# Performance work log

Hardware: AMD Instinct MI355X
Metric: run time of the kernel (lower is better)

Reference implementation:

```python
import jax, jax.numpy as jnp
import numpy as np

NEG_SLOPE = 0.2


def gat_conv(x, src, dst, W, asrc, adst, b):
    """Single-head PyG-style GATConv with self-loops.
    x: [N, din], src/dst: [E] int, W: [din, d], asrc/adst: [d], b: [d]."""
    N = x.shape[0]
    h = x @ W  # [N, d]
    alpha_s = h @ asrc  # [N]
    alpha_d = h @ adst  # [N]
    # add self loops so every node has at least one incoming edge
    loop = jnp.arange(N, dtype=src.dtype)
    srcf = jnp.concatenate([src, loop])
    dstf = jnp.concatenate([dst, loop])
    e = jax.nn.leaky_relu(alpha_s[srcf] + alpha_d[dstf], NEG_SLOPE)  # [E+N]
    m = jax.ops.segment_max(e, dstf, num_segments=N)
    ex = jnp.exp(e - m[dstf])
    denom = jax.ops.segment_sum(ex, dstf, num_segments=N)
    alpha = ex / denom[dstf]
    out = jax.ops.segment_sum(h[srcf] * alpha[:, None], dstf, num_segments=N)
    return out + b


def sdgnn_forward(x, edges, Wg, a_src, a_dst, bg, W1, b1, W2, b2):
    L = Wg.shape[0]
    R = Wg.shape[1]
    for l in range(L):
        feats = [x]
        for r in range(R):
            feats.append(gat_conv(x, edges[r, 0], edges[r, 1],
                                  Wg[l, r], a_src[l, r], a_dst[l, r], bg[l, r]))
        combined = jnp.concatenate(feats, axis=1)  # [N, 5*d]
        x = jnp.tanh(combined @ W1[l] + b1[l]) @ W2[l] + b2[l]
    return x


def setup_inputs() -> dict:
    key = jax.random.key(0)
    ks = jax.random.split(key, 8)
    N, D, E, L, R = 100000, 64, 1000000, 2, 4
    scale = 0.15  # ~kaiming for d=64
    x = jax.random.normal(ks[0], (N, D), dtype=jnp.float32)
    edges = jax.random.randint(ks[1], (R, 2, E), 0, N, dtype=jnp.int64)
    Wg = jax.random.normal(ks[2], (L, R, D, D), dtype=jnp.float32) * scale
    a_src = jax.random.normal(ks[3], (L, R, D), dtype=jnp.float32) * scale
    a_dst = jax.random.normal(ks[4], (L, R, D), dtype=jnp.float32) * scale
    bg = jnp.zeros((L, R, D), dtype=jnp.float32)
    W1 = jax.random.normal(ks[5], (L, 5 * D, D), dtype=jnp.float32) * 0.08
    b1 = jnp.zeros((L, D), dtype=jnp.float32)
    W2 = jax.random.normal(ks[6], (L, D, D), dtype=jnp.float32) * scale
    b2 = jnp.zeros((L, D), dtype=jnp.float32)
    return {"x": x, "edges": edges, "Wg": Wg, "a_src": a_src, "a_dst": a_dst,
            "bg": bg, "W1": W1, "b1": b1, "W2": W2, "b2": b2}


def reference(x, edges, Wg, a_src, a_dst, bg, W1, b1, W2, b2):
    return sdgnn_forward(x, edges, Wg, a_src, a_dst, bg, W1, b1, W2, b2)
```

## Files before the change

kernel.cpp:

```cpp
#include <hip/hip_runtime.h>
#include <hip/hip_bf16.h>
#include <math.h>

#define DD 64
#define RREL 4
#define LLAY 2
#define NEG_SLOPE 0.2f
#define EPB 4096
#define BSH 10
#define BSZ 1024

typedef __attribute__((ext_vector_type(8))) short short8;
typedef __attribute__((ext_vector_type(4))) short short4v;
typedef __attribute__((ext_vector_type(4))) float float4v;

__device__ __forceinline__ float lrelu(float x) { return x > 0.f ? x : NEG_SLOPE * x; }

__device__ __forceinline__ unsigned short f2bf(float f) {
    unsigned int u = __float_as_uint(f);
    return (unsigned short)((u + 0x7FFFu + ((u >> 16) & 1u)) >> 16);
}
__device__ __forceinline__ float bf2f(unsigned short u) {
    return __uint_as_float((unsigned int)u << 16);
}

__global__ void k_wvec(const float* __restrict__ Wg, const float* __restrict__ asrc,
                       const float* __restrict__ adst, float* __restrict__ wsrc,
                       float* __restrict__ wdst) {
    int idx = blockIdx.x * blockDim.x + threadIdx.x;
    if (idx >= LLAY * RREL * DD) return;
    int k = idx & 63;
    int lr = idx >> 6;
    const float* W = Wg + (size_t)lr * DD * DD;
    const float* as = asrc + lr * DD;
    const float* ad = adst + lr * DD;
    float s1 = 0.f, s2 = 0.f;
#pragma unroll
    for (int j = 0; j < DD; j++) {
        float w = W[k * DD + j];
        s1 += w * as[j];
        s2 += w * ad[j];
    }
    wsrc[idx] = s1;
    wdst[idx] = s2;
}

__global__ void k_prep(const float* __restrict__ Wg, const float* __restrict__ W1,
                       const float* __restrict__ W2, unsigned short* __restrict__ WgT,
                       unsigned short* __restrict__ W1T, unsigned short* __restrict__ W2T) {
    int idx = blockIdx.x * blockDim.x + threadIdx.x;
    if (idx < 8 * 4096) {
        int lr = idx >> 12, rem = idx & 4095, n = rem >> 6, k = rem & 63;
        WgT[idx] = f2bf(Wg[(size_t)lr * 4096 + k * 64 + n]);
    } else if (idx < 32768 + 2 * 64 * 320) {
        int i = idx - 32768;
        int l = i / 20480, rem = i % 20480, n = rem / 320, kk = rem % 320;
        int src;
        if (kk < 64) src = kk;
        else {
            int r = (kk - 64) >> 6, f = (kk - 64) & 63;
            src = 64 + r * 64 + ((f & 3) * 16) + (f >> 2);
        }
        W1T[i] = f2bf(W1[(size_t)l * 20480 + src * 64 + n]);
    } else if (idx < 32768 + 40960 + 2 * 4096) {
        int i = idx - 73728;
        int l = i >> 12, rem = i & 4095, n = rem >> 6, k = rem & 63;
        W2T[i] = f2bf(W2[(size_t)l * 4096 + k * 64 + n]);
    }
}

__global__ void k_copy_x(const float* __restrict__ x, unsigned short* __restrict__ combined,
                         int N) {
    int i = blockIdx.x * blockDim.x + threadIdx.x;
    if (i >= N * 32) return;
    int row = i >> 5, c2 = i & 31;
    float2 v = *(const float2*)(x + (size_t)row * DD + c2 * 2);
    unsigned int p = (unsigned int)f2bf(v.x) | ((unsigned int)f2bf(v.y) << 16);
    *(unsigned int*)(combined + (size_t)row * 320 + c2 * 2) = p;
}

__global__ void k_zero(int* __restrict__ p, int n) {
    int i = blockIdx.x * blockDim.x + threadIdx.x;
    if (i < n) p[i] = 0;
}

__global__ __launch_bounds__(256) void k_bhist(const int* __restrict__ edges,
                                               int* __restrict__ btot, int E, int NB) {
    int r = blockIdx.y;
    int e0 = blockIdx.x * EPB;
    int t = threadIdx.x;
    __shared__ int lh[128];
    for (int i = t; i < 128; i += 256) lh[i] = 0;
    __syncthreads();
    const int* dstp = edges + (size_t)r * 2 * E + E;
#pragma unroll
    for (int i = 0; i < EPB / 256; i++) {
        int e = e0 + t + 256 * i;
        if (e < E) atomicAdd(&lh[dstp[e] >> BSH], 1);
    }
    __syncthreads();
    for (int i = t; i < NB; i += 256) {
        int c = lh[i];
        if (c) atomicAdd(&btot[r * NB + i], c);
    }
}

__global__ void k_bscan(const int* __restrict__ btot, int* __restrict__ bucketoff,
                        int* __restrict__ bpos, int* __restrict__ csr_ptr, int N, int E, int NB) {
    int r = threadIdx.x;
    if (r >= RREL) return;
    int run = 0;
    for (int b = 0; b < NB; b++) {
        bucketoff[r * (NB + 1) + b] = run;
        bpos[r * NB + b] = run;
        run += btot[r * NB + b];
    }
    bucketoff[r * (NB + 1) + NB] = run;
    csr_ptr[(size_t)r * (N + 1) + N] = E;
}

__global__ __launch_bounds__(256) void k_binscatter(const int* __restrict__ edges,
                                                    int* __restrict__ bpos,
                                                    unsigned int* __restrict__ packed, int E,
                                                    int NB) {
    int r = blockIdx.y;
    int e0 = blockIdx.x * EPB;
    int t = threadIdx.x;
    __shared__ int lh[128], lbase[128];
    for (int i = t; i < 128; i += 256) lh[i] = 0;
    __syncthreads();
    const int* srcp = edges + (size_t)r * 2 * E;
    const int* dstp = srcp + E;
    int md[EPB / 256], ms[EPB / 256];
#pragma unroll
    for (int i = 0; i < EPB / 256; i++) {
        int e = e0 + t + 256 * i;
        int d = -1, s = 0;
        if (e < E) {
            d = dstp[e];
            s = srcp[e];
            atomicAdd(&lh[d >> BSH], 1);
        }
        md[i] = d;
        ms[i] = s;
    }
    __syncthreads();
    for (int i = t; i < NB; i += 256) {
        int c = lh[i];
        lbase[i] = c ? atomicAdd(&bpos[r * NB + i], c) : 0;
        lh[i] = 0;
    }
    __syncthreads();
#pragma unroll
    for (int i = 0; i < EPB / 256; i++) {
        if (md[i] >= 0) {
            int b = md[i] >> BSH;
            int p = lbase[b] + atomicAdd(&lh[b], 1);
            packed[(size_t)r * E + p] =
                ((unsigned int)(md[i] & (BSZ - 1)) << 17) | (unsigned int)ms[i];
        }
    }
}

__global__ __launch_bounds__(256) void k_bucket_sort(const unsigned int* __restrict__ packed,
                                                     const int* __restrict__ bucketoff,
                                                     int* __restrict__ csr_ptr,
                                                     int* __restrict__ csr_src, int N, int E,
                                                     int NB) {
    int r = blockIdx.y, b = blockIdx.x;
    int t = threadIdx.x;
    __shared__ int pos[BSZ];
    __shared__ int tsum[256];
    int base = bucketoff[r * (NB + 1) + b];
    int cnt = bucketoff[r * (NB + 1) + b + 1] - base;
    const unsigned int* pk = packed + (size_t)r * E + base;
    for (int i = t; i < BSZ; i += 256) pos[i] = 0;
    __syncthreads();
    for (int i = t; i < cnt; i += 256) atomicAdd(&pos[pk[i] >> 17], 1);
    __syncthreads();
    int v[4];
    int s = 0;
#pragma unroll
    for (int i = 0; i < 4; i++) {
        v[i] = pos[t * 4 + i];
        s += v[i];
    }
    tsum[t] = s;
    __syncthreads();
    for (int off = 1; off < 256; off <<= 1) {
        int add = (t >= off) ? tsum[t - off] : 0;
        __syncthreads();
        tsum[t] += add;
        __syncthreads();
    }
    int run = tsum[t] - s;
    __syncthreads();
#pragma unroll
    for (int i = 0; i < 4; i++) {
        int node_l = t * 4 + i;
        pos[node_l] = run;
        int node = b * BSZ + node_l;
        if (node < N) csr_ptr[(size_t)r * (N + 1) + node] = base + run;
        run += v[i];
    }
    __syncthreads();
    for (int i = t; i < cnt; i += 256) {
        unsigned int p = pk[i];
        int d = p >> 17;
        int sidx = p & 0x1FFFF;
        int loc = atomicAdd(&pos[d], 1);
        csr_src[(size_t)r * E + base + loc] = sidx;
    }
}

__global__ __launch_bounds__(256) void k_elog(const int* __restrict__ csr_src,
                                              const float* __restrict__ as4,
                                              float* __restrict__ e_edge, int E, int N) {
    int r = blockIdx.y;
    const int* cs = csr_src + (size_t)r * E;
    const float* as_ = as4 + (size_t)r * N;
    float* ee = e_edge + (size_t)r * E;
    int base = blockIdx.x * 1024 + threadIdx.x;
    int s[4];
#pragma unroll
    for (int u = 0; u < 4; u++) {
        int e = base + u * 256;
        s[u] = (e < E) ? cs[e] : 0;
    }
#pragma unroll
    for (int u = 0; u < 4; u++) {
        int e = base + u * 256;
        if (e < E) ee[e] = as_[s[u]];
    }
}


__global__ __launch_bounds__(256, 3) void k_hgemm(const unsigned short* __restrict__ X,
                                                  const unsigned short* __restrict__ WgTl,
                                                  const float* __restrict__ wsrcl,
                                                  const float* __restrict__ wdstl,
                                                  unsigned short* __restrict__ h4,
                                                  float* __restrict__ as4,
                                                  float* __restrict__ ad4, int N) {
    __shared__ __align__(16) unsigned short Xb[256][72];
    __shared__ __align__(16) unsigned short Wb[64][72];
    __shared__ float wsS[4][64], wdS[4][64];
    int tid = threadIdx.x, wave = tid >> 6, lane = tid & 63;
    int l15 = lane & 15, q = lane >> 4;
    int row0 = blockIdx.x * 256;
#pragma unroll
    for (int i = 0; i < 8; i++) {
        int f = tid + 256 * i;
        int rr = f >> 3, seg = f & 7;
        int grow = row0 + rr;
        short8 v = (short8){0, 0, 0, 0, 0, 0, 0, 0};
        if (grow < N) v = *(const short8*)(X + (size_t)grow * 320 + seg * 8);
        *(short8*)&Xb[rr][seg * 8] = v;
    }
    wsS[tid >> 6][tid & 63] = wsrcl[tid];
    wdS[tid >> 6][tid & 63] = wdstl[tid];
    __syncthreads();
    short8 afr[4][2];
#pragma unroll
    for (int mt = 0; mt < 4; mt++)
#pragma unroll
        for (int ks = 0; ks < 2; ks++)
            afr[mt][ks] = *(const short8*)&Xb[wave * 64 + mt * 16 + l15][ks * 32 + q * 8];
    {
        int grow = row0 + tid;
        float s[4] = {0.f, 0.f, 0.f, 0.f}, d[4] = {0.f, 0.f, 0.f, 0.f};
#pragma unroll
        for (int seg = 0; seg < 8; seg++) {
            short8 v = *(const short8*)&Xb[tid][seg * 8];
#pragma unroll
            for (int j = 0; j < 8; j++) {
                float xv = bf2f((unsigned short)v[j]);
                int k = seg * 8 + j;
#pragma unroll
                for (int r = 0; r < 4; r++) {
                    s[r] += xv * wsS[r][k];
                    d[r] += xv * wdS[r][k];
                }
            }
        }
        if (grow < N) {
#pragma unroll
            for (int r = 0; r < 4; r++) {
                as4[(size_t)r * N + grow] = s[r];
                ad4[(size_t)r * N + grow] = d[r];
            }
        }
    }
    for (int r = 0; r < 4; r++) {
        __syncthreads();
#pragma unroll
        for (int i = 0; i < 2; i++) {
            int f = tid + 256 * i;
            int n = f >> 3, seg = f & 7;
            *(short8*)&Wb[n][seg * 8] = *(const short8*)(WgTl + r * 4096 + n * 64 + seg * 8);
        }
        __syncthreads();
        short8 bfr[4][2];
#pragma unroll
        for (int nt = 0; nt < 4; nt++)
#pragma unroll
            for (int ks = 0; ks < 2; ks++)
                bfr[nt][ks] = *(const short8*)&Wb[nt * 16 + l15][ks * 32 + q * 8];
        float4v acc[4][4];
#pragma unroll
        for (int mt = 0; mt < 4; mt++)
#pragma unroll
            for (int nt = 0; nt < 4; nt++) acc[mt][nt] = (float4v){0.f, 0.f, 0.f, 0.f};
#pragma unroll
        for (int mt = 0; mt < 4; mt++)
#pragma unroll
            for (int nt = 0; nt < 4; nt++) {
                acc[mt][nt] = __builtin_amdgcn_mfma_f32_16x16x32_bf16(afr[mt][0], bfr[nt][0],
                                                                     acc[mt][nt], 0, 0, 0);
                acc[mt][nt] = __builtin_amdgcn_mfma_f32_16x16x32_bf16(afr[mt][1], bfr[nt][1],
                                                                     acc[mt][nt], 0, 0, 0);
            }
        unsigned short* hr = h4 + (size_t)r * N * 64;
#pragma unroll
        for (int mt = 0; mt < 4; mt++) {
            int rowb = row0 + wave * 64 + mt * 16 + q * 4;
#pragma unroll
            for (int reg = 0; reg < 4; reg++) {
                int row = rowb + reg;
                if (row < N) {
                    short4v sv;
                    sv[0] = (short)f2bf(acc[mt][0][reg]);
                    sv[1] = (short)f2bf(acc[mt][1][reg]);
                    sv[2] = (short)f2bf(acc[mt][2][reg]);
                    sv[3] = (short)f2bf(acc[mt][3][reg]);
                    *(short4v*)&hr[(size_t)row * 64 + l15 * 4] = sv;
                }
            }
        }
    }
}

__global__ __launch_bounds__(256, 3) void k_w1gemm(const unsigned short* __restrict__ X,
                                                   const unsigned short* __restrict__ WT,
                                                   const float* __restrict__ bias,
                                                   unsigned short* __restrict__ Y, int N) {
    __shared__ __align__(16) unsigned short Xb[256][72];
    __shared__ __align__(16) unsigned short Wb[64][72];
    int tid = threadIdx.x, wave = tid >> 6, lane = tid & 63;
    int l15 = lane & 15, q = lane >> 4;
    int row0 = blockIdx.x * 256;
    float4v acc[4][4];
#pragma unroll
    for (int mt = 0; mt < 4; mt++)
#pragma unroll
        for (int nt = 0; nt < 4; nt++) acc[mt][nt] = (float4v){0.f, 0.f, 0.f, 0.f};
    for (int kc = 0; kc < 320; kc += 64) {
        __syncthreads();
#pragma unroll
        for (int i = 0; i < 8; i++) {
            int f = tid + 256 * i;
            int rr = f >> 3, seg = f & 7;
            int grow = row0 + rr;
            short8 v = (short8){0, 0, 0, 0, 0, 0, 0, 0};
            if (grow < N) v = *(const short8*)(X + (size_t)grow * 320 + kc + seg * 8);
            *(short8*)&Xb[rr][seg * 8] = v;
        }
#pragma unroll
        for (int i = 0; i < 2; i++) {
            int f = tid + 256 * i;
            int n = f >> 3, seg = f & 7;
            *(short8*)&Wb[n][seg * 8] = *(const short8*)(WT + n * 320 + kc + seg * 8);
        }
        __syncthreads();
        short8 bfr[4][2];
#pragma unroll
        for (int nt = 0; nt < 4; nt++)
#pragma unroll
            for (int ks = 0; ks < 2; ks++)
                bfr[nt][ks] = *(const short8*)&Wb[nt * 16 + l15][ks * 32 + q * 8];
#pragma unroll
        for (int mt = 0; mt < 4; mt++) {
            short8 a0 = *(const short8*)&Xb[wave * 64 + mt * 16 + l15][q * 8];
            short8 a1 = *(const short8*)&Xb[wave * 64 + mt * 16 + l15][32 + q * 8];
#pragma unroll
            for (int nt = 0; nt < 4; nt++) {
                acc[mt][nt] =
                    __builtin_amdgcn_mfma_f32_16x16x32_bf16(a0, bfr[nt][0], acc[mt][nt], 0, 0, 0);
                acc[mt][nt] =
                    __builtin_amdgcn_mfma_f32_16x16x32_bf16(a1, bfr[nt][1], acc[mt][nt], 0, 0, 0);
            }
        }
    }
#pragma unroll
    for (int mt = 0; mt < 4; mt++) {
        int rowb = row0 + wave * 64 + mt * 16 + q * 4;
#pragma unroll
        for (int reg = 0; reg < 4; reg++) {
            int row = rowb + reg;
            if (row < N) {
#pragma unroll
                for (int nt = 0; nt < 4; nt++) {
                    int n = nt * 16 + l15;
                    float v = tanhf(acc[mt][nt][reg] + bias[n]);
                    Y[(size_t)row * 64 + n] = f2bf(v);
                }
            }
        }
    }
}

template <bool BFOUT>
__global__ __launch_bounds__(256, 3) void k_w2gemm(const unsigned short* __restrict__ X,
                                                   const unsigned short* __restrict__ WT,
                                                   const float* __restrict__ bias,
                                                   unsigned short* __restrict__ Ybf,
                                                   float* __restrict__ Yf, int ldy, int N) {
    __shared__ __align__(16) unsigned short Xb[256][72];
    __shared__ __align__(16) unsigned short Wb[64][72];
    int tid = threadIdx.x, wave = tid >> 6, lane = tid & 63;
    int l15 = lane & 15, q = lane >> 4;
    int row0 = blockIdx.x * 256;
#pragma unroll
    for (int i = 0; i < 8; i++) {
        int f = tid + 256 * i;
        int rr = f >> 3, seg = f & 7;
        int grow = row0 + rr;
        short8 v = (short8){0, 0, 0, 0, 0, 0, 0, 0};
        if (grow < N) v = *(const short8*)(X + (size_t)grow * 64 + seg * 8);
        *(short8*)&Xb[rr][seg * 8] = v;
    }
#pragma unroll
    for (int i = 0; i < 2; i++) {
        int f = tid + 256 * i;
        int n = f >> 3, seg = f & 7;
        *(short8*)&Wb[n][seg * 8] = *(const short8*)(WT + n * 64 + seg * 8);
    }
    __syncthreads();
    short8 bfr[4][2];
#pragma unroll
    for (int nt = 0; nt < 4; nt++)
#pragma unroll
        for (int ks = 0; ks < 2; ks++)
            bfr[nt][ks] = *(const short8*)&Wb[nt * 16 + l15][ks * 32 + q * 8];
    float4v acc[4][4];
#pragma unroll
    for (int mt = 0; mt < 4; mt++)
#pragma unroll
        for (int nt = 0; nt < 4; nt++) acc[mt][nt] = (float4v){0.f, 0.f, 0.f, 0.f};
#pragma unroll
    for (int mt = 0; mt < 4; mt++) {
        short8 a0 = *(const short8*)&Xb[wave * 64 + mt * 16 + l15][q * 8];
        short8 a1 = *(const short8*)&Xb[wave * 64 + mt * 16 + l15][32 + q * 8];
#pragma unroll
        for (int nt = 0; nt < 4; nt++) {
            acc[mt][nt] =
                __builtin_amdgcn_mfma_f32_16x16x32_bf16(a0, bfr[nt][0], acc[mt][nt], 0, 0, 0);
            acc[mt][nt] =
                __builtin_amdgcn_mfma_f32_16x16x32_bf16(a1, bfr[nt][1], acc[mt][nt], 0, 0, 0);
        }
    }
#pragma unroll
    for (int mt = 0; mt < 4; mt++) {
        int rowb = row0 + wave * 64 + mt * 16 + q * 4;
#pragma unroll
        for (int reg = 0; reg < 4; reg++) {
            int row = rowb + reg;
            if (row < N) {
#pragma unroll
                for (int nt = 0; nt < 4; nt++) {
                    int n = nt * 16 + l15;
                    float v = acc[mt][nt][reg] + bias[n];
                    if (BFOUT)
                        Ybf[(size_t)row * ldy + n] = f2bf(v);
                    else
                        Yf[(size_t)row * ldy + n] = v;
                }
            }
        }
    }
}

__device__ void gat_node_fullwave(int node, const int* __restrict__ csr_ptr,
                                  const int* __restrict__ csr_src,
                                  const float* __restrict__ e_edge,
                                  const unsigned short* __restrict__ h,
                                  const float* __restrict__ as_,
                                  const float* __restrict__ ad_, float bgv,
                                  unsigned short* __restrict__ out, int ldo, int lane) {
    float adv = ad_[node];
    float e_self = lrelu(as_[node] + adv);
    int beg = csr_ptr[node], end = csr_ptr[node + 1];
    int cnt = end - beg;

    if (cnt <= 64) {
        int s = 0;
        float e_lane = -3.0e38f;
        if (lane < cnt) {
            s = csr_src[beg + lane];
            e_lane = lrelu(e_edge[beg + lane] + adv);
        }
        float m = fmaxf(e_lane, e_self);
#pragma unroll
        for (int off = 32; off; off >>= 1) m = fmaxf(m, __shfl_xor(m, off));
        float p = (lane < cnt) ? expf(e_lane - m) : 0.f;
        float ssum = p;
#pragma unroll
        for (int off = 32; off; off >>= 1) ssum += __shfl_xor(ssum, off);
        float p_self = expf(e_self - m);
        float inv = 1.f / (ssum + p_self);
        float alpha = p * inv;
        float acc = p_self * inv * bf2f(h[(size_t)node * DD + lane]);
        for (int j0 = 0; j0 < cnt; ++j0) {
            int ss = __shfl(s, j0);
            float aa = __shfl(alpha, j0);
            acc += aa * bf2f(h[(size_t)ss * DD + lane]);
        }
        out[(size_t)node * ldo + lane] = f2bf(acc + bgv);
        return;
    }

    float m = e_self;
    for (int j = beg + lane; j < end; j += 64) m = fmaxf(m, lrelu(e_edge[j] + adv));
#pragma unroll
    for (int off = 32; off; off >>= 1) m = fmaxf(m, __shfl_xor(m, off));
    float ssum = 0.f;
    for (int j = beg + lane; j < end; j += 64) ssum += expf(lrelu(e_edge[j] + adv) - m);
#pragma unroll
    for (int off = 32; off; off >>= 1) ssum += __shfl_xor(ssum, off);
    ssum += expf(e_self - m);
    float inv = 1.f / ssum;
    float acc = expf(e_self - m) * inv * bf2f(h[(size_t)node * DD + lane]);
    for (int j0 = beg; j0 < end; j0 += 64) {
        int j = j0 + lane;
        int s = 0;
        float alpha = 0.f;
        if (j < end) {
            s = csr_src[j];
            alpha = expf(lrelu(e_edge[j] + adv) - m) * inv;
        }
        int c = end - j0;
        if (c > 64) c = 64;
        for (int t = 0; t < c; ++t) {
            int ss = __shfl(s, t);
            float aa = __shfl(alpha, t);
            acc += aa * bf2f(h[(size_t)ss * DD + lane]);
        }
    }
    out[(size_t)node * ldo + lane] = f2bf(acc + bgv);
}

__global__ __launch_bounds__(256) void k_gat(const int* __restrict__ csr_ptr4,
                                             const int* __restrict__ csr_src4,
                                             const float* __restrict__ e_edge4,
                                             const unsigned short* __restrict__ h4,
                                             const float* __restrict__ as4,
                                             const float* __restrict__ ad4,
                                             const float* __restrict__ bg4,
                                             unsigned short* __restrict__ outbase, int ldo,
                                             int N, int E) {
    __shared__ int2 lsa[4][2][32];
    int lb = blockIdx.x;
    int r = (lb & 7) >> 1;
    int idx = ((lb >> 3) << 1) + (lb & 1);
    int wave = threadIdx.x >> 6, lane = threadIdx.x & 63;
    int half = lane >> 5, lh = lane & 31;
    int nodeA = idx * 8 + wave * 2;
    if (nodeA >= N) return;
    int node = nodeA + half;
    bool act = node < N;

    const int* csr_ptr = csr_ptr4 + (size_t)r * (N + 1);
    const int* csr_src = csr_src4 + (size_t)r * E;
    const float* e_edge = e_edge4 + (size_t)r * E;
    const unsigned short* h = h4 + (size_t)r * N * 64;
    const float* as_ = as4 + (size_t)r * N;
    const float* ad_ = ad4 + (size_t)r * N;
    const float* bg = bg4 + (size_t)r * DD;
    unsigned short* out = outbase + (size_t)64 * r;

    int beg = 0, cnt = 0;
    if (act) {
        beg = csr_ptr[node];
        cnt = csr_ptr[node + 1] - beg;
    }
    int vmax = __builtin_amdgcn_readfirstlane(max(cnt, __shfl_xor(cnt, 32)));

    if (vmax <= 32) {
        bool in = lh < cnt;
        int s = 0;
        float ev = 0.f;
        if (in) {
            s = csr_src[beg + lh];
            ev = e_edge[beg + lh];
        }
        float adv = act ? ad_[node] : 0.f;
        float e_self = act ? lrelu(as_[node] + adv) : 0.f;
        float p = in ? __expf(lrelu(ev + adv)) : 0.f;
        lsa[wave][half][lh] = make_int2(s, __float_as_int(p));
        float p_self = __expf(e_self);

        const char* hb = (const char*)h;
        unsigned lane4 = (unsigned)(lh << 2);
        unsigned int hvs = 0;
        if (act) hvs = *(const unsigned int*)(hb + (((unsigned)node) << 7) + lane4);

        float ax0 = 0.f, ay0 = 0.f, ax1 = 0.f, ay1 = 0.f;
        const int2* lp = &lsa[wave][half][0];
        for (int j0 = 0; j0 < vmax; j0 += 8) {
#pragma unroll
            for (int g = 0; g < 2; g++) {
                if (j0 + g * 4 < vmax) {
#pragma unroll
                    for (int u = 0; u < 4; u++) {
                        int2 sa = lp[j0 + g * 4 + u];
                        unsigned voff = ((unsigned)sa.x << 7) + lane4;
                        unsigned int hv = *(const unsigned int*)(hb + voff);
                        float pw = __int_as_float(sa.y);
                        if (u & 1) {
                            ax1 += pw * __uint_as_float(hv << 16);
                            ay1 += pw * __uint_as_float(hv & 0xffff0000u);
                        } else {
                            ax0 += pw * __uint_as_float(hv << 16);
                            ay0 += pw * __uint_as_float(hv & 0xffff0000u);
                        }
                    }
                }
            }
        }
        float ssum = p;
#pragma unroll
        for (int off = 16; off; off >>= 1) ssum += __shfl_xor(ssum, off);
        float inv = __builtin_amdgcn_rcpf(ssum + p_self);

        if (act) {
            int f0 = 2 * lh;
            float bx = bg[((f0 & 3) << 4) | (f0 >> 2)];
            float by = bg[(((f0 + 1) & 3) << 4) | (f0 >> 2)];
            float ox = (ax0 + ax1 + p_self * __uint_as_float(hvs << 16)) * inv + bx;
            float oy = (ay0 + ay1 + p_self * __uint_as_float(hvs & 0xffff0000u)) * inv + by;
            unsigned int pck = (unsigned int)f2bf(ox) | ((unsigned int)f2bf(oy) << 16);
            *(unsigned int*)(out + (size_t)node * ldo + f0) = pck;
        }
        return;
    }

    float bgv = bg[((lane & 3) << 4) | (lane >> 2)];
    if (nodeA < N)
        gat_node_fullwave(nodeA, csr_ptr, csr_src, e_edge, h, as_, ad_, bgv, out, ldo, lane);
    if (nodeA + 1 < N)
        gat_node_fullwave(nodeA + 1, csr_ptr, csr_src, e_edge, h, as_, ad_, bgv, out, ldo, lane);
}

extern "C" void kernel_launch(void* const* d_in, const int* in_sizes, int n_in,
                              void* d_out, int out_size, void* d_ws, size_t ws_size,
                              hipStream_t stream) {
    const float* x = (const float*)d_in[0];
    const int* edges = (const int*)d_in[1];
    const float* Wg = (const float*)d_in[2];
    const float* a_src = (const float*)d_in[3];
    const float* a_dst = (const float*)d_in[4];
    const float* bg = (const float*)d_in[5];
    const float* W1 = (const float*)d_in[6];
    const float* b1 = (const float*)d_in[7];
    const float* W2 = (const float*)d_in[8];
    const float* b2 = (const float*)d_in[9];
    float* out = (float*)d_out;

    const int N = in_sizes[0] / DD;
    const int E = in_sizes[1] / (2 * RREL);
    const int NB = (N + BSZ - 1) >> BSH;

    size_t off = 0;
    auto alloc = [&](size_t bytes) {
        size_t o = off;
        off = (off + bytes + 255) & ~(size_t)255;
        return o;
    };
    char* ws = (char*)d_ws;
    unsigned short* combined = (unsigned short*)(ws + alloc((size_t)N * 320 * 2));
    unsigned short* h4 = (unsigned short*)(ws + alloc((size_t)4 * N * 64 * 2));
    float* wsrc = (float*)(ws + alloc(LLAY * RREL * DD * 4));
    float* wdst = (float*)(ws + alloc(LLAY * RREL * DD * 4));
    unsigned short* WgT = (unsigned short*)(ws + alloc(8 * 4096 * 2));
    unsigned short* W1T = (unsigned short*)(ws + alloc(2 * 64 * 320 * 2));
    unsigned short* W2T = (unsigned short*)(ws + alloc(2 * 4096 * 2));
    int* btot = (int*)(ws + alloc((size_t)RREL * NB * 4));
    int* bucketoff = (int*)(ws + alloc((size_t)RREL * (NB + 1) * 4));
    int* bpos = (int*)(ws + alloc((size_t)RREL * NB * 4));
    unsigned int* packed = (unsigned int*)(ws + alloc((size_t)RREL * E * 4));
    int* csr_ptr = (int*)(ws + alloc((size_t)RREL * (N + 1) * 4));
    int* csr_src = (int*)(ws + alloc((size_t)RREL * E * 4));
    float* e_edge = (float*)(ws + alloc((size_t)RREL * E * 4));
    (void)ws_size;
    unsigned short* hid = h4;
    float* as4 = (float*)packed;
    float* ad4 = as4 + (size_t)4 * N;

    const int ebblocks = (E + EPB - 1) / EPB;

    k_zero<<<dim3((RREL * NB + 255) / 256), dim3(256), 0, stream>>>(btot, RREL * NB);
    k_wvec<<<dim3(2), dim3(256), 0, stream>>>(Wg, a_src, a_dst, wsrc, wdst);
    k_prep<<<dim3(320), dim3(256), 0, stream>>>(Wg, W1, W2, WgT, W1T, W2T);
    k_copy_x<<<dim3((N * 32 + 255) / 256), dim3(256), 0, stream>>>(x, combined, N);
    k_bhist<<<dim3(ebblocks, RREL), dim3(256), 0, stream>>>(edges, btot, E, NB);
    k_bscan<<<dim3(1), dim3(64), 0, stream>>>(btot, bucketoff, bpos, csr_ptr, N, E, NB);
    k_binscatter<<<dim3(ebblocks, RREL), dim3(256), 0, stream>>>(edges, bpos, packed, E, NB);
    k_bucket_sort<<<dim3(NB, RREL), dim3(256), 0, stream>>>(packed, bucketoff, csr_ptr, csr_src,
                                                            N, E, NB);

    const int gemm_blocks = (N + 255) / 256;
    const int elog_blocks = (E + 1023) / 1024;
    const int bpr = (N + 7) / 8;
    const int gat_grid = 8 * ((bpr + 1) / 2);

    for (int l = 0; l < LLAY; l++) {
        k_hgemm<<<dim3(gemm_blocks), dim3(256), 0, stream>>>(
            combined, WgT + (size_t)l * 4 * 4096, wsrc + l * 256, wdst + l * 256, h4, as4, ad4, N);
        k_elog<<<dim3(elog_blocks, RREL), dim3(256), 0, stream>>>(csr_src, as4, e_edge, E, N);
        k_gat<<<dim3(gat_grid), dim3(256), 0, stream>>>(
            csr_ptr, csr_src, e_edge, h4, as4, ad4, bg + (size_t)l * RREL * DD,
            combined + 64, 320, N, E);
        k_w1gemm<<<dim3(gemm_blocks), dim3(256), 0, stream>>>(combined, W1T + (size_t)l * 20480,
                                                              b1 + l * DD, hid, N);
        if (l == LLAY - 1) {
            k_w2gemm<false><<<dim3(gemm_blocks), dim3(256), 0, stream>>>(
                hid, W2T + (size_t)l * 4096, b2 + l * DD, nullptr, out, DD, N);
        } else {
            k_w2gemm<true><<<dim3(gemm_blocks), dim3(256), 0, stream>>>(
                hid, W2T + (size_t)l * 4096, b2 + l * DD, combined, nullptr, 320, N);
        }
    }
}
```

Measured before the change: 562.3 us.

## Fuse edge-logit gather into GAT kernel and merge W1/W2 GEMMs into one MLP kernel

Removes the separate edge-logit kernel and its per-edge buffer, so the GAT kernel gathers source attention scores directly through csr_src. The W1 GEMM and the W2 GEMM become one kernel that keeps the tanh hidden tile in shared memory, so the hidden activations never go to global memory. Both changes cut a launch and a full global write-and-read pass per layer. The cost is extra random gathers in the GAT inner loop, plus recomputing those gathers across the max and sum passes for high-degree nodes.

```diff
diff --git a/kernel.cpp b/kernel.cpp
--- a/kernel.cpp
+++ b/kernel.cpp
@@ -213,27 +213,6 @@
     }
 }
 
-__global__ __launch_bounds__(256) void k_elog(const int* __restrict__ csr_src,
-                                              const float* __restrict__ as4,
-                                              float* __restrict__ e_edge, int E, int N) {
-    int r = blockIdx.y;
-    const int* cs = csr_src + (size_t)r * E;
-    const float* as_ = as4 + (size_t)r * N;
-    float* ee = e_edge + (size_t)r * E;
-    int base = blockIdx.x * 1024 + threadIdx.x;
-    int s[4];
-#pragma unroll
-    for (int u = 0; u < 4; u++) {
-        int e = base + u * 256;
-        s[u] = (e < E) ? cs[e] : 0;
-    }
-#pragma unroll
-    for (int u = 0; u < 4; u++) {
-        int e = base + u * 256;
-        if (e < E) ee[e] = as_[s[u]];
-    }
-}
-
 
 __global__ __launch_bounds__(256, 3) void k_hgemm(const unsigned short* __restrict__ X,
                                                   const unsigned short* __restrict__ WgTl,
@@ -340,10 +319,14 @@
     }
 }
 
-__global__ __launch_bounds__(256, 3) void k_w1gemm(const unsigned short* __restrict__ X,
-                                                   const unsigned short* __restrict__ WT,
-                                                   const float* __restrict__ bias,
-                                                   unsigned short* __restrict__ Y, int N) {
+template <bool BFOUT>
+__global__ __launch_bounds__(256, 3) void k_mlp(const unsigned short* __restrict__ X,
+                                                const unsigned short* __restrict__ W1Tl,
+                                                const float* __restrict__ b1,
+                                                const unsigned short* __restrict__ W2Tl,
+                                                const float* __restrict__ b2,
+                                                unsigned short* __restrict__ Ybf,
+                                                float* __restrict__ Yf, int ldy, int N) {
     __shared__ __align__(16) unsigned short Xb[256][72];
     __shared__ __align__(16) unsigned short Wb[64][72];
     int tid = threadIdx.x, wave = tid >> 6, lane = tid & 63;
@@ -369,7 +352,7 @@
         for (int i = 0; i < 2; i++) {
             int f = tid + 256 * i;
             int n = f >> 3, seg = f & 7;
-            *(short8*)&Wb[n][seg * 8] = *(const short8*)(WT + n * 320 + kc + seg * 8);
+            *(short8*)&Wb[n][seg * 8] = *(const short8*)(W1Tl + n * 320 + kc + seg * 8);
         }
         __syncthreads();
         short8 bfr[4][2];
@@ -391,6 +374,49 @@
             }
         }
     }
+    __syncthreads();
+#pragma unroll
+    for (int mt = 0; mt < 4; mt++) {
+        int rlb = wave * 64 + mt * 16 + q * 4;
+#pragma unroll
+        for (int reg = 0; reg < 4; reg++) {
+#pragma unroll
+            for (int nt = 0; nt < 4; nt++) {
+                int n = nt * 16 + l15;
+                Xb[rlb + reg][n] = f2bf(tanhf(acc[mt][nt][reg] + b1[n]));
+            }
+        }
+    }
+#pragma unroll
+    for (int i = 0; i < 2; i++) {
+        int f = tid + 256 * i;
+        int n = f >> 3, seg = f & 7;
+        *(short8*)&Wb[n][seg * 8] = *(const short8*)(W2Tl + n * 64 + seg * 8);
+    }
+    __syncthreads();
+    short8 bfr[4][2];
+#pragma unroll
+    for (int nt = 0; nt < 4; nt++)
+#pragma unroll
+        for (int ks = 0; ks < 2; ks++)
+            bfr[nt][ks] = *(const short8*)&Wb[nt * 16 + l15][ks * 32 + q * 8];
+    float4v acc2[4][4];
+#pragma unroll
+    for (int mt = 0; mt < 4; mt++)
+#pragma unroll
+        for (int nt = 0; nt < 4; nt++) acc2[mt][nt] = (float4v){0.f, 0.f, 0.f, 0.f};
+#pragma unroll
+    for (int mt = 0; mt < 4; mt++) {
+        short8 a0 = *(const short8*)&Xb[wave * 64 + mt * 16 + l15][q * 8];
+        short8 a1 = *(const short8*)&Xb[wave * 64 + mt * 16 + l15][32 + q * 8];
+#pragma unroll
+        for (int nt = 0; nt < 4; nt++) {
+            acc2[mt][nt] =
+                __builtin_amdgcn_mfma_f32_16x16x32_bf16(a0, bfr[nt][0], acc2[mt][nt], 0, 0, 0);
+            acc2[mt][nt] =
+                __builtin_amdgcn_mfma_f32_16x16x32_bf16(a1, bfr[nt][1], acc2[mt][nt], 0, 0, 0);
+        }
+    }
 #pragma unroll
     for (int mt = 0; mt < 4; mt++) {
         int rowb = row0 + wave * 64 + mt * 16 + q * 4;
@@ -401,75 +427,7 @@
 #pragma unroll
                 for (int nt = 0; nt < 4; nt++) {
                     int n = nt * 16 + l15;
-                    float v = tanhf(acc[mt][nt][reg] + bias[n]);
-                    Y[(size_t)row * 64 + n] = f2bf(v);
-                }
-            }
-        }
-    }
-}
-
-template <bool BFOUT>
-__global__ __launch_bounds__(256, 3) void k_w2gemm(const unsigned short* __restrict__ X,
-                                                   const unsigned short* __restrict__ WT,
-                                                   const float* __restrict__ bias,
-                                                   unsigned short* __restrict__ Ybf,
-                                                   float* __restrict__ Yf, int ldy, int N) {
-    __shared__ __align__(16) unsigned short Xb[256][72];
-    __shared__ __align__(16) unsigned short Wb[64][72];
-    int tid = threadIdx.x, wave = tid >> 6, lane = tid & 63;
-    int l15 = lane & 15, q = lane >> 4;
-    int row0 = blockIdx.x * 256;
-#pragma unroll
-    for (int i = 0; i < 8; i++) {
-        int f = tid + 256 * i;
-        int rr = f >> 3, seg = f & 7;
-        int grow = row0 + rr;
-        short8 v = (short8){0, 0, 0, 0, 0, 0, 0, 0};
-        if (grow < N) v = *(const short8*)(X + (size_t)grow * 64 + seg * 8);
-        *(short8*)&Xb[rr][seg * 8] = v;
-    }
-#pragma unroll
-    for (int i = 0; i < 2; i++) {
-        int f = tid + 256 * i;
-        int n = f >> 3, seg = f & 7;
-        *(short8*)&Wb[n][seg * 8] = *(const short8*)(WT + n * 64 + seg * 8);
-    }
-    __syncthreads();
-    short8 bfr[4][2];
-#pragma unroll
-    for (int nt = 0; nt < 4; nt++)
-#pragma unroll
-        for (int ks = 0; ks < 2; ks++)
-            bfr[nt][ks] = *(const short8*)&Wb[nt * 16 + l15][ks * 32 + q * 8];
-    float4v acc[4][4];
-#pragma unroll
-    for (int mt = 0; mt < 4; mt++)
-#pragma unroll
-        for (int nt = 0; nt < 4; nt++) acc[mt][nt] = (float4v){0.f, 0.f, 0.f, 0.f};
-#pragma unroll
-    for (int mt = 0; mt < 4; mt++) {
-        short8 a0 = *(const short8*)&Xb[wave * 64 + mt * 16 + l15][q * 8];
-        short8 a1 = *(const short8*)&Xb[wave * 64 + mt * 16 + l15][32 + q * 8];
-#pragma unroll
-        for (int nt = 0; nt < 4; nt++) {
-            acc[mt][nt] =
-                __builtin_amdgcn_mfma_f32_16x16x32_bf16(a0, bfr[nt][0], acc[mt][nt], 0, 0, 0);
-            acc[mt][nt] =
-                __builtin_amdgcn_mfma_f32_16x16x32_bf16(a1, bfr[nt][1], acc[mt][nt], 0, 0, 0);
-        }
-    }
-#pragma unroll
-    for (int mt = 0; mt < 4; mt++) {
-        int rowb = row0 + wave * 64 + mt * 16 + q * 4;
-#pragma unroll
-        for (int reg = 0; reg < 4; reg++) {
-            int row = rowb + reg;
-            if (row < N) {
-#pragma unroll
-                for (int nt = 0; nt < 4; nt++) {
-                    int n = nt * 16 + l15;
-                    float v = acc[mt][nt][reg] + bias[n];
+                    float v = acc2[mt][nt][reg] + b2[n];
                     if (BFOUT)
                         Ybf[(size_t)row * ldy + n] = f2bf(v);
                     else
@@ -482,7 +440,6 @@
 
 __device__ void gat_node_fullwave(int node, const int* __restrict__ csr_ptr,
                                   const int* __restrict__ csr_src,
-                                  const float* __restrict__ e_edge,
                                   const unsigned short* __restrict__ h,
                                   const float* __restrict__ as_,
                                   const float* __restrict__ ad_, float bgv,
@@ -497,7 +454,7 @@
         float e_lane = -3.0e38f;
         if (lane < cnt) {
             s = csr_src[beg + lane];
-            e_lane = lrelu(e_edge[beg + lane] + adv);
+            e_lane = lrelu(as_[s] + adv);
         }
         float m = fmaxf(e_lane, e_self);
 #pragma unroll
@@ -520,11 +477,11 @@
     }
 
     float m = e_self;
-    for (int j = beg + lane; j < end; j += 64) m = fmaxf(m, lrelu(e_edge[j] + adv));
+    for (int j = beg + lane; j < end; j += 64) m = fmaxf(m, lrelu(as_[csr_src[j]] + adv));
 #pragma unroll
     for (int off = 32; off; off >>= 1) m = fmaxf(m, __shfl_xor(m, off));
     float ssum = 0.f;
-    for (int j = beg + lane; j < end; j += 64) ssum += expf(lrelu(e_edge[j] + adv) - m);
+    for (int j = beg + lane; j < end; j += 64) ssum += expf(lrelu(as_[csr_src[j]] + adv) - m);
 #pragma unroll
     for (int off = 32; off; off >>= 1) ssum += __shfl_xor(ssum, off);
     ssum += expf(e_self - m);
@@ -536,7 +493,7 @@
         float alpha = 0.f;
         if (j < end) {
             s = csr_src[j];
-            alpha = expf(lrelu(e_edge[j] + adv) - m) * inv;
+            alpha = expf(lrelu(as_[s] + adv) - m) * inv;
         }
         int c = end - j0;
         if (c > 64) c = 64;
@@ -551,14 +508,14 @@
 
 __global__ __launch_bounds__(256) void k_gat(const int* __restrict__ csr_ptr4,
                                              const int* __restrict__ csr_src4,
-                                             const float* __restrict__ e_edge4,
                                              const unsigned short* __restrict__ h4,
                                              const float* __restrict__ as4,
                                              const float* __restrict__ ad4,
                                              const float* __restrict__ bg4,
                                              unsigned short* __restrict__ outbase, int ldo,
                                              int N, int E) {
-    __shared__ int2 lsa[4][2][32];
+    __shared__ int lsa_s[4][2][32];
+    __shared__ float lsa_p[4][2][32];
     int lb = blockIdx.x;
     int r = (lb & 7) >> 1;
     int idx = ((lb >> 3) << 1) + (lb & 1);
@@ -571,7 +528,6 @@
 
     const int* csr_ptr = csr_ptr4 + (size_t)r * (N + 1);
     const int* csr_src = csr_src4 + (size_t)r * E;
-    const float* e_edge = e_edge4 + (size_t)r * E;
     const unsigned short* h = h4 + (size_t)r * N * 64;
     const float* as_ = as4 + (size_t)r * N;
     const float* ad_ = ad4 + (size_t)r * N;
@@ -588,15 +544,13 @@
     if (vmax <= 32) {
         bool in = lh < cnt;
         int s = 0;
-        float ev = 0.f;
-        if (in) {
-            s = csr_src[beg + lh];
-            ev = e_edge[beg + lh];
-        }
+        if (in) s = csr_src[beg + lh];
+        lsa_s[wave][half][lh] = s;
         float adv = act ? ad_[node] : 0.f;
+        float asl = in ? as_[s] : 0.f;
         float e_self = act ? lrelu(as_[node] + adv) : 0.f;
-        float p = in ? __expf(lrelu(ev + adv)) : 0.f;
-        lsa[wave][half][lh] = make_int2(s, __float_as_int(p));
+        float p = in ? __expf(lrelu(asl + adv)) : 0.f;
+        lsa_p[wave][half][lh] = p;
         float p_self = __expf(e_self);
 
         const char* hb = (const char*)h;
@@ -605,17 +559,18 @@
         if (act) hvs = *(const unsigned int*)(hb + (((unsigned)node) << 7) + lane4);
 
         float ax0 = 0.f, ay0 = 0.f, ax1 = 0.f, ay1 = 0.f;
-        const int2* lp = &lsa[wave][half][0];
+        const int* sp = &lsa_s[wave][half][0];
+        const float* pp = &lsa_p[wave][half][0];
         for (int j0 = 0; j0 < vmax; j0 += 8) {
 #pragma unroll
             for (int g = 0; g < 2; g++) {
                 if (j0 + g * 4 < vmax) {
 #pragma unroll
                     for (int u = 0; u < 4; u++) {
-                        int2 sa = lp[j0 + g * 4 + u];
-                        unsigned voff = ((unsigned)sa.x << 7) + lane4;
+                        int sv = sp[j0 + g * 4 + u];
+                        unsigned voff = ((unsigned)sv << 7) + lane4;
                         unsigned int hv = *(const unsigned int*)(hb + voff);
-                        float pw = __int_as_float(sa.y);
+                        float pw = pp[j0 + g * 4 + u];
                         if (u & 1) {
                             ax1 += pw * __uint_as_float(hv << 16);
                             ay1 += pw * __uint_as_float(hv & 0xffff0000u);
@@ -646,9 +601,9 @@
 
     float bgv = bg[((lane & 3) << 4) | (lane >> 2)];
     if (nodeA < N)
-        gat_node_fullwave(nodeA, csr_ptr, csr_src, e_edge, h, as_, ad_, bgv, out, ldo, lane);
+        gat_node_fullwave(nodeA, csr_ptr, csr_src, h, as_, ad_, bgv, out, ldo, lane);
     if (nodeA + 1 < N)
-        gat_node_fullwave(nodeA + 1, csr_ptr, csr_src, e_edge, h, as_, ad_, bgv, out, ldo, lane);
+        gat_node_fullwave(nodeA + 1, csr_ptr, csr_src, h, as_, ad_, bgv, out, ldo, lane);
 }
 
 extern "C" void kernel_launch(void* const* d_in, const int* in_sizes, int n_in,
@@ -690,9 +645,7 @@
     unsigned int* packed = (unsigned int*)(ws + alloc((size_t)RREL * E * 4));
     int* csr_ptr = (int*)(ws + alloc((size_t)RREL * (N + 1) * 4));
     int* csr_src = (int*)(ws + alloc((size_t)RREL * E * 4));
-    float* e_edge = (float*)(ws + alloc((size_t)RREL * E * 4));
     (void)ws_size;
-    unsigned short* hid = h4;
     float* as4 = (float*)packed;
     float* ad4 = as4 + (size_t)4 * N;
 
@@ -709,25 +662,23 @@
                                                             N, E, NB);
 
     const int gemm_blocks = (N + 255) / 256;
-    const int elog_blocks = (E + 1023) / 1024;
     const int bpr = (N + 7) / 8;
     const int gat_grid = 8 * ((bpr + 1) / 2);
 
     for (int l = 0; l < LLAY; l++) {
         k_hgemm<<<dim3(gemm_blocks), dim3(256), 0, stream>>>(
             combined, WgT + (size_t)l * 4 * 4096, wsrc + l * 256, wdst + l * 256, h4, as4, ad4, N);
-        k_elog<<<dim3(elog_blocks, RREL), dim3(256), 0, stream>>>(csr_src, as4, e_edge, E, N);
         k_gat<<<dim3(gat_grid), dim3(256), 0, stream>>>(
-            csr_ptr, csr_src, e_edge, h4, as4, ad4, bg + (size_t)l * RREL * DD,
+            csr_ptr, csr_src, h4, as4, ad4, bg + (size_t)l * RREL * DD,
             combined + 64, 320, N, E);
-        k_w1gemm<<<dim3(gemm_blocks), dim3(256), 0, stream>>>(combined, W1T + (size_t)l * 20480,
-                                                              b1 + l * DD, hid, N);
         if (l == LLAY - 1) {
-            k_w2gemm<false><<<dim3(gemm_blocks), dim3(256), 0, stream>>>(
-                hid, W2T + (size_t)l * 4096, b2 + l * DD, nullptr, out, DD, N);
+            k_mlp<false><<<dim3(gemm_blocks), dim3(256), 0, stream>>>(
+                combined, W1T + (size_t)l * 20480, b1 + l * DD, W2T + (size_t)l * 4096,
+                b2 + l * DD, nullptr, out, DD, N);
         } else {
-            k_w2gemm<true><<<dim3(gemm_blocks), dim3(256), 0, stream>>>(
-                hid, W2T + (size_t)l * 4096, b2 + l * DD, combined, nullptr, 320, N);
-        }
-    }
-}
+            k_mlp<true><<<dim3(gemm_blocks), dim3(256), 0, stream>>>(
+                combined, W1T + (size_t)l * 20480, b1 + l * DD, W2T + (size_t)l * 4096,
+                b2 + l * DD, combined, nullptr, 320, N);
+        }
+    }
+}
```

After: 504.3 us. 10.3% less time.
